# Performance work log

Hardware: AMD Instinct MI355X
Metric: run time of the kernel (lower is better)

The kernel has to match this reference:

```python
import jax, jax.numpy as jnp
import numpy as np


def setup_inputs() -> dict:
    key = jax.random.key(0)
    k1, k2, k3 = jax.random.split(key, 3)
    L, B, H = 256, 8, 512
    inputs = jax.random.normal(k1, (L, B, H), dtype=jnp.float32)
    attn_W = jax.random.normal(k2, (H, 2 * H), dtype=jnp.float32) * 0.02
    attn_b = jnp.zeros((H,), dtype=jnp.float32)
    score_W = jax.random.normal(k3, (1, H), dtype=jnp.float32) * 0.02
    score_b = jnp.zeros((1,), dtype=jnp.float32)
    return {"inputs": inputs, "attn_W": attn_W, "attn_b": attn_b,
            "score_W": score_W, "score_b": score_b}


def reference(inputs, attn_W, attn_b, score_W, score_b):
    # inputs: [L, B, H]; attn_W: [H, 2H] (torch Linear weight), attn_b: [H]
    # score_W: [1, H], score_b: [1]
    H = attn_W.shape[0]
    # Decompose Linear(cat(sen1, sen2)) = sen1 @ W1^T + sen2 @ W2^T + b
    W1 = attn_W[:, :H]   # [H, H] acts on sen1 (row index i)
    W2 = attn_W[:, H:]   # [H, H] acts on sen2 (col index j)
    x = jnp.transpose(inputs, (1, 0, 2))          # [B, L, H]
    p1 = jnp.einsum('blh,oh->blo', x, W1)         # [B, L, H]
    p2 = jnp.einsum('blh,oh->blo', x, W2)         # [B, L, H]
    # feat[b,i,j,:] = tanh(attn(cat(x[b,i], x[b,j])))  -> [B, L, L, H]
    feat = jnp.tanh(p1[:, :, None, :] + p2[:, None, :, :] + attn_b)
    # score Linear H -> 1, squeeze last dim -> [B, L, L]
    energies = jnp.einsum('bijh,h->bij', feat, score_W[0]) + score_b[0]
    # softmax over dim=1 (the sen1 / i axis), as in the torch code
    return jax.nn.softmax(energies, axis=1)
```

## Files before the change

kernel.cpp:

```cpp
#include <hip/hip_runtime.h>

#define LOG2E 1.4426950408889634f
#define SCALE (2.0f * LOG2E)

__device__ __forceinline__ float fast_exp2(float x) { return __builtin_amdgcn_exp2f(x); }
__device__ __forceinline__ float fast_rcp(float x)  { return __builtin_amdgcn_rcpf(x); }

typedef __attribute__((ext_vector_type(8))) short bf16x8;
typedef __attribute__((ext_vector_type(4))) float f32x4;

__global__ __launch_bounds__(256) void pack_kernel(const float* __restrict__ inputs,
                                                   const float* __restrict__ attn_W,
                                                   ushort* __restrict__ Ap,
                                                   ushort* __restrict__ Bp) {
    int tid = blockIdx.x * 256 + threadIdx.x;
    const bool isA = tid < 393216;
    int f = isA ? tid : tid - 393216;
    int l  = f & 63;
    int fr = (f >> 6) & 3;
    int ks = (f >> 8) & 1;
    int rem = f >> 9;
    int kt = rem % 24, tb = rem / 24;
    int kp = kt * 64 + ks * 32 + (l >> 4) * 8;
    int seg = kp >> 9, k = kp & 511;
    const float* src;
    bool useLo;
    if (isA) {
        int m = tb * 64 + fr * 16 + (l & 15);
        src = inputs + ((m & 255) * 8 + (m >> 8)) * 512 + k;
        useLo = (seg == 1);
    } else {
        int n = tb * 64 + fr * 16 + (l & 15);
        src = attn_W + (n & 511) * 1024 + (n >> 9) * 512 + k;
        useLo = (seg == 2);
    }
    float4 v0 = *(const float4*)src;
    float4 v1 = *(const float4*)(src + 4);
    float vv[8] = {v0.x, v0.y, v0.z, v0.w, v1.x, v1.y, v1.z, v1.w};
    ushort o[8];
#pragma unroll
    for (int j = 0; j < 8; ++j) {
        unsigned u = __float_as_uint(vv[j]);
        unsigned hi = (u + 0x7FFF + ((u >> 16) & 1)) >> 16;
        if (useLo) {
            float lo = vv[j] - __uint_as_float(hi << 16);
            unsigned ul = __float_as_uint(lo);
            o[j] = (ushort)((ul + 0x7FFF + ((ul >> 16) & 1)) >> 16);
        } else {
            o[j] = (ushort)hi;
        }
    }
    ushort* dst = (isA ? Ap : Bp) + (long)f * 8;
    *(uint4*)dst = *(const uint4*)o;
}

__global__ __launch_bounds__(256) void mfma_gemm(const ushort* __restrict__ Ap,
                                                 const ushort* __restrict__ Bp,
                                                 const float* __restrict__ attn_b,
                                                 float* __restrict__ E1,
                                                 float* __restrict__ E2) {
    const int mb = blockIdx.x & 15;
    const int nb = blockIdx.x >> 4;
    __shared__ ushort lds[2][12288];

    const int t = threadIdx.x;
    const int lane = t & 63, w = t >> 6;
    const int wr = w >> 1, wc = w & 1;

    const ushort* A0 = Ap + (long)(mb * 2 + 0) * 24 * 4096;
    const ushort* A1 = Ap + (long)(mb * 2 + 1) * 24 * 4096;
    const ushort* B0 = Bp + (long)nb * 24 * 4096;

    f32x4 acc[4][2];
#pragma unroll
    for (int i = 0; i < 4; ++i)
#pragma unroll
        for (int j = 0; j < 2; ++j)
            acc[i][j] = (f32x4){0.f, 0.f, 0.f, 0.f};

    uint4 st[6];
    st[0] = ((const uint4*)A0)[t];       st[1] = ((const uint4*)A0)[t + 256];
    st[2] = ((const uint4*)A1)[t];       st[3] = ((const uint4*)A1)[t + 256];
    st[4] = ((const uint4*)B0)[t];       st[5] = ((const uint4*)B0)[t + 256];
#pragma unroll
    for (int r = 0; r < 6; ++r) ((uint4*)lds[0])[t + r * 256] = st[r];
    __syncthreads();

    for (int kt = 0; kt < 24; ++kt) {
        if (kt < 23) {
            const uint4* a0 = (const uint4*)(A0 + (kt + 1) * 4096);
            const uint4* a1 = (const uint4*)(A1 + (kt + 1) * 4096);
            const uint4* b0 = (const uint4*)(B0 + (kt + 1) * 4096);
            st[0] = a0[t]; st[1] = a0[t + 256];
            st[2] = a1[t]; st[3] = a1[t + 256];
            st[4] = b0[t]; st[5] = b0[t + 256];
        }
        const ushort* buf = lds[kt & 1];
#pragma unroll
        for (int ks = 0; ks < 2; ++ks) {
            bf16x8 a[4], b[2];
#pragma unroll
            for (int mf = 0; mf < 4; ++mf)
                a[mf] = *(const bf16x8*)&buf[wr * 4096 + ks * 2048 + mf * 512 + lane * 8];
#pragma unroll
            for (int nn = 0; nn < 2; ++nn)
                b[nn] = *(const bf16x8*)&buf[8192 + ks * 2048 + (wc * 2 + nn) * 512 + lane * 8];
#pragma unroll
            for (int mf = 0; mf < 4; ++mf)
#pragma unroll
                for (int nn = 0; nn < 2; ++nn)
                    acc[mf][nn] = __builtin_amdgcn_mfma_f32_16x16x32_bf16(
                        a[mf], b[nn], acc[mf][nn], 0, 0, 0);
        }
        if (kt < 23) {
            ushort* nbuf = lds[(kt + 1) & 1];
#pragma unroll
            for (int r = 0; r < 6; ++r) ((uint4*)nbuf)[t + r * 256] = st[r];
            __syncthreads();
        }
    }

    const bool isE1 = (nb < 8);
    float* dst = isE1 ? E1 : E2;
    const int b = mb >> 1;
#pragma unroll
    for (int nn = 0; nn < 2; ++nn) {
        int n = nb * 64 + wc * 32 + nn * 16 + (lane & 15);
        int o = n & 511;
        float bias = isE1 ? attn_b[o] : 0.0f;
#pragma unroll
        for (int mf = 0; mf < 4; ++mf) {
            int ti = (mb & 1) * 4 + wr * 2 + (mf >> 1);
            int iibase = (mf & 1) * 16 + (lane >> 4) * 4;
            long rowoff = ((long)(b * 8 + ti) * 512 + o) * 32 + iibase;
#pragma unroll
            for (int r = 0; r < 4; ++r)
                dst[rowoff + r] = fast_exp2(SCALE * (acc[mf][nn][r] + bias));
        }
    }
}

__global__ __launch_bounds__(256) void energy_kernel(const float* __restrict__ E1,
                                                     const float* __restrict__ E2,
                                                     const float* __restrict__ sW,
                                                     float* __restrict__ EP) {
    const int bid = blockIdx.x;
    const int s  = bid & 3;
    const int tj = (bid >> 2) & 7;
    const int ti = (bid >> 5) & 7;
    const int b  = bid >> 8;
    __shared__ float p1s[64 * 32];
    __shared__ float p2s[64 * 32];
    __shared__ float csh[128];

    const int t = threadIdx.x;
    const int tx = t & 15, ty = t >> 4;

    if (t < 128) csh[t] = 2.0f * sW[s * 128 + t];

    const float* p1base = E1 + ((long)(b * 8 + ti) * 512 + s * 128) * 32;
    const float* p2base = E2 + ((long)(b * 8 + tj) * 512 + s * 128) * 32;

    float acc00 = 0.f, acc01 = 0.f, acc10 = 0.f, acc11 = 0.f;

    for (int c0 = 0; c0 < 128; c0 += 64) {
        __syncthreads();
        const float4* s1 = (const float4*)(p1base + c0 * 32);
        const float4* s2 = (const float4*)(p2base + c0 * 32);
        float4* d1 = (float4*)p1s;
        float4* d2 = (float4*)p2s;
        d1[t] = s1[t];  d1[256 + t] = s1[256 + t];
        d2[t] = s2[t];  d2[256 + t] = s2[256 + t];
        __syncthreads();
#pragma unroll 8
        for (int hh = 0; hh < 64; ++hh) {
            float c = csh[c0 + hh];
            float2 a  = *(const float2*)&p1s[hh * 32 + ty * 2];
            float2 bj = *(const float2*)&p2s[hh * 32 + tx * 2];
            acc00 = fmaf(c, fast_rcp(fmaf(a.x, bj.x, 1.0f)), acc00);
            acc01 = fmaf(c, fast_rcp(fmaf(a.x, bj.y, 1.0f)), acc01);
            acc10 = fmaf(c, fast_rcp(fmaf(a.y, bj.x, 1.0f)), acc10);
            acc11 = fmaf(c, fast_rcp(fmaf(a.y, bj.y, 1.0f)), acc11);
        }
    }

    float* Eb = EP + (long)s * 524288 + (long)b * 65536 + (ti * 32) * 256 + tj * 32;
    *(float2*)&Eb[(ty * 2 + 0) * 256 + tx * 2] = make_float2(acc00, acc01);
    *(float2*)&Eb[(ty * 2 + 1) * 256 + tx * 2] = make_float2(acc10, acc11);
}

__global__ __launch_bounds__(256) void softmax_kernel(const float* __restrict__ P0,
                                                      const float* __restrict__ P1,
                                                      const float* __restrict__ P2,
                                                      const float* __restrict__ P3,
                                                      float* __restrict__ out) {
    const int b  = blockIdx.x >> 4;
    const int jt = blockIdx.x & 15;
    const int t  = threadIdx.x;
    const int jx = t & 15;
    const int iy = t >> 4;
    const long base = (long)b * 65536 + jt * 16 + jx;

    float v[16];
#pragma unroll
    for (int k = 0; k < 16; ++k) {
        long idx = base + (long)(iy + k * 16) * 256;
        v[k] = -(P0[idx] + P1[idx] + P2[idx] + P3[idx]);
    }

    float m = v[0];
#pragma unroll
    for (int k = 1; k < 16; ++k) m = fmaxf(m, v[k]);

    __shared__ float red[256];
    red[t] = m;
    __syncthreads();
    if (t < 128) red[t] = fmaxf(red[t], red[t + 128]);
    __syncthreads();
    if (t < 64) red[t] = fmaxf(red[t], red[t + 64]);
    __syncthreads();
    if (t < 32) red[t] = fmaxf(red[t], red[t + 32]);
    __syncthreads();
    if (t < 16) red[t] = fmaxf(red[t], red[t + 16]);
    __syncthreads();
    m = red[jx];
    __syncthreads();

    float ssum = 0.f;
#pragma unroll
    for (int k = 0; k < 16; ++k) {
        v[k] = fast_exp2((v[k] - m) * LOG2E);
        ssum += v[k];
    }
    red[t] = ssum;
    __syncthreads();
    if (t < 128) red[t] += red[t + 128];
    __syncthreads();
    if (t < 64) red[t] += red[t + 64];
    __syncthreads();
    if (t < 32) red[t] += red[t + 32];
    __syncthreads();
    if (t < 16) red[t] += red[t + 16];
    __syncthreads();
    float inv = fast_rcp(red[jx]);

#pragma unroll
    for (int k = 0; k < 16; ++k) {
        long idx = base + (long)(iy + k * 16) * 256;
        out[idx] = v[k] * inv;
    }
}

extern "C" void kernel_launch(void* const* d_in, const int* in_sizes, int n_in,
                              void* d_out, int out_size, void* d_ws, size_t ws_size,
                              hipStream_t stream) {
    const float* inputs  = (const float*)d_in[0];
    const float* attn_W  = (const float*)d_in[1];
    const float* attn_b  = (const float*)d_in[2];
    const float* score_W = (const float*)d_in[3];
    float* out = (float*)d_out;

    float* ws = (float*)d_ws;
    float* E1 = ws;
    float* E2 = ws + (1 << 20);
    float* EP = ws + (2 << 20);
    ushort* Ap = (ushort*)(ws + (4 << 20));
    ushort* Bp = Ap + 3145728;

    pack_kernel<<<2304, 256, 0, stream>>>(inputs, attn_W, Ap, Bp);
    mfma_gemm<<<256, 256, 0, stream>>>(Ap, Bp, attn_b, E1, E2);
    energy_kernel<<<2048, 256, 0, stream>>>(E1, E2, score_W, EP);
    softmax_kernel<<<128, 256, 0, stream>>>(EP, EP + 524288, EP + 2 * 524288,
                                            EP + 3 * 524288, out);
}
```

Before: 64.23 us.

## Combine four reciprocals into one in energy kernel with larger 4x4 register tiles

The energy kernel now puts four rational terms c/(1+ab) over a common denominator, so each group of four hidden units needs a single reciprocal instead of four. It also computes a 4x4 output micro-tile per thread with packed float2 math. Shared memory is transposed and padded, and the hidden dimension is split into 8 partial slices instead of 4, which means the softmax kernel now sums 8 partial buffers. The aim is to ease the transcendental-unit bottleneck, with the risks of possible overflow or precision loss in the product denominators and more partial-sum traffic.

```diff
diff --git a/kernel.cpp b/kernel.cpp
--- a/kernel.cpp
+++ b/kernel.cpp
@@ -8,6 +8,8 @@
 
 typedef __attribute__((ext_vector_type(8))) short bf16x8;
 typedef __attribute__((ext_vector_type(4))) float f32x4;
+typedef __attribute__((ext_vector_type(2))) float f32x2;
+#define F2(u,v) ((f32x2){(u),(v)})
 
 __global__ __launch_bounds__(256) void pack_kernel(const float* __restrict__ inputs,
                                                    const float* __restrict__ attn_W,
@@ -145,54 +147,88 @@
                                                      const float* __restrict__ sW,
                                                      float* __restrict__ EP) {
     const int bid = blockIdx.x;
-    const int s  = bid & 3;
-    const int tj = (bid >> 2) & 7;
-    const int ti = (bid >> 5) & 7;
-    const int b  = bid >> 8;
-    __shared__ float p1s[64 * 32];
-    __shared__ float p2s[64 * 32];
-    __shared__ float csh[128];
+    const int tj = bid & 3;
+    const int ti = (bid >> 2) & 3;
+    const int b  = (bid >> 4) & 7;
+    const int s  = bid >> 7;
+    __shared__ float As[64 * 33];
+    __shared__ float Bs[64 * 33];
+    __shared__ float csh[64];
 
     const int t = threadIdx.x;
     const int tx = t & 15, ty = t >> 4;
-
-    if (t < 128) csh[t] = 2.0f * sW[s * 128 + t];
-
-    const float* p1base = E1 + ((long)(b * 8 + ti) * 512 + s * 128) * 32;
-    const float* p2base = E2 + ((long)(b * 8 + tj) * 512 + s * 128) * 32;
-
-    float acc00 = 0.f, acc01 = 0.f, acc10 = 0.f, acc11 = 0.f;
-
-    for (int c0 = 0; c0 < 128; c0 += 64) {
+    if (t < 64) csh[t] = 2.0f * sW[s * 64 + t];
+
+    const int oo = t & 31, iig = t >> 5;
+    const float* a_src = E1 + (long)(b * 8 + ti * 2 + (iig >> 2)) * 16384 + (iig & 3) * 8;
+    const float* b_src = E2 + (long)(b * 8 + tj * 2 + (iig >> 2)) * 16384 + (iig & 3) * 8;
+
+    f32x2 acc[4][2];
+#pragma unroll
+    for (int r = 0; r < 4; ++r)
+#pragma unroll
+        for (int cp = 0; cp < 2; ++cp) acc[r][cp] = F2(0.f, 0.f);
+
+    const f32x2 one = F2(1.f, 1.f);
+
+    for (int st = 0; st < 2; ++st) {
+        const long ob = (long)(s * 64 + st * 32 + oo) * 32;
+        float4 va0 = *(const float4*)(a_src + ob);
+        float4 va1 = *(const float4*)(a_src + ob + 4);
+        float4 vb0 = *(const float4*)(b_src + ob);
+        float4 vb1 = *(const float4*)(b_src + ob + 4);
         __syncthreads();
-        const float4* s1 = (const float4*)(p1base + c0 * 32);
-        const float4* s2 = (const float4*)(p2base + c0 * 32);
-        float4* d1 = (float4*)p1s;
-        float4* d2 = (float4*)p2s;
-        d1[t] = s1[t];  d1[256 + t] = s1[256 + t];
-        d2[t] = s2[t];  d2[256 + t] = s2[256 + t];
+        const int di = iig * 8;
+        As[(di + 0) * 33 + oo] = va0.x; As[(di + 1) * 33 + oo] = va0.y;
+        As[(di + 2) * 33 + oo] = va0.z; As[(di + 3) * 33 + oo] = va0.w;
+        As[(di + 4) * 33 + oo] = va1.x; As[(di + 5) * 33 + oo] = va1.y;
+        As[(di + 6) * 33 + oo] = va1.z; As[(di + 7) * 33 + oo] = va1.w;
+        Bs[(di + 0) * 33 + oo] = vb0.x; Bs[(di + 1) * 33 + oo] = vb0.y;
+        Bs[(di + 2) * 33 + oo] = vb0.z; Bs[(di + 3) * 33 + oo] = vb0.w;
+        Bs[(di + 4) * 33 + oo] = vb1.x; Bs[(di + 5) * 33 + oo] = vb1.y;
+        Bs[(di + 6) * 33 + oo] = vb1.z; Bs[(di + 7) * 33 + oo] = vb1.w;
         __syncthreads();
-#pragma unroll 8
-        for (int hh = 0; hh < 64; ++hh) {
-            float c = csh[c0 + hh];
-            float2 a  = *(const float2*)&p1s[hh * 32 + ty * 2];
-            float2 bj = *(const float2*)&p2s[hh * 32 + tx * 2];
-            acc00 = fmaf(c, fast_rcp(fmaf(a.x, bj.x, 1.0f)), acc00);
-            acc01 = fmaf(c, fast_rcp(fmaf(a.x, bj.y, 1.0f)), acc01);
-            acc10 = fmaf(c, fast_rcp(fmaf(a.y, bj.x, 1.0f)), acc10);
-            acc11 = fmaf(c, fast_rcp(fmaf(a.y, bj.y, 1.0f)), acc11);
-        }
-    }
-
-    float* Eb = EP + (long)s * 524288 + (long)b * 65536 + (ti * 32) * 256 + tj * 32;
-    *(float2*)&Eb[(ty * 2 + 0) * 256 + tx * 2] = make_float2(acc00, acc01);
-    *(float2*)&Eb[(ty * 2 + 1) * 256 + tx * 2] = make_float2(acc10, acc11);
-}
-
-__global__ __launch_bounds__(256) void softmax_kernel(const float* __restrict__ P0,
-                                                      const float* __restrict__ P1,
-                                                      const float* __restrict__ P2,
-                                                      const float* __restrict__ P3,
+
+#pragma unroll
+        for (int g = 0; g < 8; ++g) {
+            float4 c4 = *(const float4*)&csh[st * 32 + g * 4];
+            float4 av[4], bv[4];
+#pragma unroll
+            for (int r = 0; r < 4; ++r)
+                av[r] = *(const float4*)&As[(ty * 4 + r) * 33 + g * 4];
+#pragma unroll
+            for (int c = 0; c < 4; ++c)
+                bv[c] = *(const float4*)&Bs[(tx * 4 + c) * 33 + g * 4];
+#pragma unroll
+            for (int r = 0; r < 4; ++r) {
+#pragma unroll
+                for (int cp = 0; cp < 2; ++cp) {
+                    const float4 B0 = bv[cp * 2], B1 = bv[cp * 2 + 1];
+                    f32x2 y0 = F2(B0.x, B1.x) * av[r].x + one;
+                    f32x2 y1 = F2(B0.y, B1.y) * av[r].y + one;
+                    f32x2 y2 = F2(B0.z, B1.z) * av[r].z + one;
+                    f32x2 y3 = F2(B0.w, B1.w) * av[r].w + one;
+                    f32x2 y01 = y0 * y1, y23 = y2 * y3;
+                    f32x2 d = y01 * y23;
+                    f32x2 n01 = y1 * c4.x + y0 * c4.y;
+                    f32x2 n23 = y3 * c4.z + y2 * c4.w;
+                    f32x2 n = n01 * y23 + n23 * y01;
+                    f32x2 rr = F2(fast_rcp(d.x), fast_rcp(d.y));
+                    acc[r][cp] += n * rr;
+                }
+            }
+        }
+    }
+
+    float* Eb = EP + (long)s * 524288 + (long)b * 65536 + (long)(ti * 64) * 256 + tj * 64;
+#pragma unroll
+    for (int r = 0; r < 4; ++r)
+#pragma unroll
+        for (int cp = 0; cp < 2; ++cp)
+            *(f32x2*)&Eb[(ty * 4 + r) * 256 + tx * 4 + cp * 2] = acc[r][cp];
+}
+
+__global__ __launch_bounds__(256) void softmax_kernel(const float* __restrict__ EP,
                                                       float* __restrict__ out) {
     const int b  = blockIdx.x >> 4;
     const int jt = blockIdx.x & 15;
@@ -205,7 +241,10 @@
 #pragma unroll
     for (int k = 0; k < 16; ++k) {
         long idx = base + (long)(iy + k * 16) * 256;
-        v[k] = -(P0[idx] + P1[idx] + P2[idx] + P3[idx]);
+        float sum = 0.f;
+#pragma unroll
+        for (int p = 0; p < 8; ++p) sum += EP[(long)p * 524288 + idx];
+        v[k] = -sum;
     }
 
     float m = v[0];
@@ -264,12 +303,11 @@
     float* E1 = ws;
     float* E2 = ws + (1 << 20);
     float* EP = ws + (2 << 20);
-    ushort* Ap = (ushort*)(ws + (4 << 20));
+    ushort* Ap = (ushort*)(ws + (6 << 20));
     ushort* Bp = Ap + 3145728;
 
     pack_kernel<<<2304, 256, 0, stream>>>(inputs, attn_W, Ap, Bp);
     mfma_gemm<<<256, 256, 0, stream>>>(Ap, Bp, attn_b, E1, E2);
-    energy_kernel<<<2048, 256, 0, stream>>>(E1, E2, score_W, EP);
-    softmax_kernel<<<128, 256, 0, stream>>>(EP, EP + 524288, EP + 2 * 524288,
-                                            EP + 3 * 524288, out);
-}
+    energy_kernel<<<1024, 256, 0, stream>>>(E1, E2, score_W, EP);
+    softmax_kernel<<<128, 256, 0, stream>>>(EP, out);
+}
```

Measured after the change: 86.56 us. 1.35x slower.

## Drop LDS staging in GEMM; stream fragments directly to registers with triple buffering

Applied to the files above, without the earlier changes.

Each wavefront in the bf16 MFMA GEMM now works independently and loads its pre-packed A and B fragments straight from global memory into registers. A three-stage register ring prefetches two k-steps ahead, replacing the shared-memory double buffer and its block barriers. The block-to-tile mapping is also remapped across the grid. This removes LDS traffic and __syncthreads stalls, but gives up reuse of tiles across wavefronts, so global and L2 load traffic goes up and register pressure rises.

```diff
diff --git a/kernel.cpp b/kernel.cpp
--- a/kernel.cpp
+++ b/kernel.cpp
@@ -59,17 +59,14 @@
                                                  const float* __restrict__ attn_b,
                                                  float* __restrict__ E1,
                                                  float* __restrict__ E2) {
-    const int mb = blockIdx.x & 15;
-    const int nb = blockIdx.x >> 4;
-    __shared__ ushort lds[2][12288];
-
-    const int t = threadIdx.x;
-    const int lane = t & 63, w = t >> 6;
-    const int wr = w >> 1, wc = w & 1;
-
-    const ushort* A0 = Ap + (long)(mb * 2 + 0) * 24 * 4096;
-    const ushort* A1 = Ap + (long)(mb * 2 + 1) * 24 * 4096;
-    const ushort* B0 = Bp + (long)nb * 24 * 4096;
+    const int lb = (blockIdx.x & 7) * 32 + (blockIdx.x >> 3);
+    const int w = (lb << 2) | (threadIdx.x >> 6);
+    const int lane = threadIdx.x & 63;
+    const int mt  = w >> 5;
+    const int nt2 = w & 31;
+
+    const ushort* pa = Ap + (long)mt * 98304 + lane * 8;
+    const ushort* pb = Bp + (long)(nt2 >> 1) * 98304 + (nt2 & 1) * 1024 + lane * 8;
 
     f32x4 acc[4][2];
 #pragma unroll
@@ -78,61 +75,49 @@
         for (int j = 0; j < 2; ++j)
             acc[i][j] = (f32x4){0.f, 0.f, 0.f, 0.f};
 
-    uint4 st[6];
-    st[0] = ((const uint4*)A0)[t];       st[1] = ((const uint4*)A0)[t + 256];
-    st[2] = ((const uint4*)A1)[t];       st[3] = ((const uint4*)A1)[t + 256];
-    st[4] = ((const uint4*)B0)[t];       st[5] = ((const uint4*)B0)[t + 256];
-#pragma unroll
-    for (int r = 0; r < 6; ++r) ((uint4*)lds[0])[t + r * 256] = st[r];
-    __syncthreads();
-
-    for (int kt = 0; kt < 24; ++kt) {
-        if (kt < 23) {
-            const uint4* a0 = (const uint4*)(A0 + (kt + 1) * 4096);
-            const uint4* a1 = (const uint4*)(A1 + (kt + 1) * 4096);
-            const uint4* b0 = (const uint4*)(B0 + (kt + 1) * 4096);
-            st[0] = a0[t]; st[1] = a0[t + 256];
-            st[2] = a1[t]; st[3] = a1[t + 256];
-            st[4] = b0[t]; st[5] = b0[t + 256];
-        }
-        const ushort* buf = lds[kt & 1];
-#pragma unroll
-        for (int ks = 0; ks < 2; ++ks) {
-            bf16x8 a[4], b[2];
-#pragma unroll
-            for (int mf = 0; mf < 4; ++mf)
-                a[mf] = *(const bf16x8*)&buf[wr * 4096 + ks * 2048 + mf * 512 + lane * 8];
+    bf16x8 bufA[3][4], bufB[3][2];
+#define LOADK(kk, s)                                              \
+    {                                                             \
+        const ushort* qa = pa + (kk) * 2048;                      \
+        const ushort* qb = pb + (kk) * 2048;                      \
+        bufA[s][0] = *(const bf16x8*)qa;                          \
+        bufA[s][1] = *(const bf16x8*)(qa + 512);                  \
+        bufA[s][2] = *(const bf16x8*)(qa + 1024);                 \
+        bufA[s][3] = *(const bf16x8*)(qa + 1536);                 \
+        bufB[s][0] = *(const bf16x8*)qb;                          \
+        bufB[s][1] = *(const bf16x8*)(qb + 512);                  \
+    }
+
+    LOADK(0, 0);
+    LOADK(1, 1);
+#pragma unroll 3
+    for (int kk = 0; kk < 48; ++kk) {
+        const int cur = kk % 3;
+        if (kk < 46) {
+            const int nxt = (kk + 2) % 3;
+            LOADK(kk + 2, nxt);
+        }
+#pragma unroll
+        for (int mf = 0; mf < 4; ++mf)
 #pragma unroll
             for (int nn = 0; nn < 2; ++nn)
-                b[nn] = *(const bf16x8*)&buf[8192 + ks * 2048 + (wc * 2 + nn) * 512 + lane * 8];
-#pragma unroll
-            for (int mf = 0; mf < 4; ++mf)
-#pragma unroll
-                for (int nn = 0; nn < 2; ++nn)
-                    acc[mf][nn] = __builtin_amdgcn_mfma_f32_16x16x32_bf16(
-                        a[mf], b[nn], acc[mf][nn], 0, 0, 0);
-        }
-        if (kt < 23) {
-            ushort* nbuf = lds[(kt + 1) & 1];
-#pragma unroll
-            for (int r = 0; r < 6; ++r) ((uint4*)nbuf)[t + r * 256] = st[r];
-            __syncthreads();
-        }
-    }
-
-    const bool isE1 = (nb < 8);
+                acc[mf][nn] = __builtin_amdgcn_mfma_f32_16x16x32_bf16(
+                    bufA[cur][mf], bufB[cur][nn], acc[mf][nn], 0, 0, 0);
+    }
+#undef LOADK
+
+    const bool isE1 = (nt2 < 16);
     float* dst = isE1 ? E1 : E2;
-    const int b = mb >> 1;
 #pragma unroll
     for (int nn = 0; nn < 2; ++nn) {
-        int n = nb * 64 + wc * 32 + nn * 16 + (lane & 15);
+        int n = nt2 * 32 + nn * 16 + (lane & 15);
         int o = n & 511;
         float bias = isE1 ? attn_b[o] : 0.0f;
 #pragma unroll
         for (int mf = 0; mf < 4; ++mf) {
-            int ti = (mb & 1) * 4 + wr * 2 + (mf >> 1);
-            int iibase = (mf & 1) * 16 + (lane >> 4) * 4;
-            long rowoff = ((long)(b * 8 + ti) * 512 + o) * 32 + iibase;
+            int ml = mt * 64 + mf * 16 + ((lane >> 4) << 2);
+            int bb = ml >> 8, l = ml & 255;
+            long rowoff = ((long)(bb * 8 + (l >> 5)) * 512 + o) * 32 + (l & 31);
 #pragma unroll
             for (int r = 0; r < 4; ++r)
                 dst[rowoff + r] = fast_exp2(SCALE * (acc[mf][nn][r] + bias));
```

New measurement: 67.57 us. 5.2% more time.

## Enlarge GEMM block tile to 256x128 with 8 waves per block

Applied to the files above, without the earlier changes.

The bf16 MFMA GEMM now uses 512-thread blocks that each compute a 256x128 output tile, instead of 256-thread blocks computing 128x64 tiles. The grid shrinks from 256 blocks to 64. Each wave accumulates a 64x64 sub-tile, which raises data reuse per LDS load and cuts the total global traffic for A and B. In exchange, only 64 blocks run on a GPU with many more compute units, so most of the device sits idle, and register and LDS use per block roughly double.

```diff
diff --git a/kernel.cpp b/kernel.cpp
--- a/kernel.cpp
+++ b/kernel.cpp
@@ -54,88 +54,97 @@
     *(uint4*)dst = *(const uint4*)o;
 }
 
-__global__ __launch_bounds__(256) void mfma_gemm(const ushort* __restrict__ Ap,
+__global__ __launch_bounds__(512) void mfma_gemm(const ushort* __restrict__ Ap,
                                                  const ushort* __restrict__ Bp,
                                                  const float* __restrict__ attn_b,
                                                  float* __restrict__ E1,
                                                  float* __restrict__ E2) {
-    const int mb = blockIdx.x & 15;
-    const int nb = blockIdx.x >> 4;
-    __shared__ ushort lds[2][12288];
+    const int mt = blockIdx.x & 7;
+    const int nb = blockIdx.x >> 3;
+    __shared__ ushort lds[2][24576];
 
     const int t = threadIdx.x;
     const int lane = t & 63, w = t >> 6;
-    const int wr = w >> 1, wc = w & 1;
-
-    const ushort* A0 = Ap + (long)(mb * 2 + 0) * 24 * 4096;
-    const ushort* A1 = Ap + (long)(mb * 2 + 1) * 24 * 4096;
-    const ushort* B0 = Bp + (long)nb * 24 * 4096;
-
-    f32x4 acc[4][2];
+    const int wrm = w >> 1, wcn = w & 1;
+
+    const ushort* aBase = Ap + (long)(mt * 4) * 98304;
+    const ushort* bBase = Bp + (long)(nb * 2) * 98304;
+
+    f32x4 acc[4][4];
 #pragma unroll
     for (int i = 0; i < 4; ++i)
 #pragma unroll
-        for (int j = 0; j < 2; ++j)
+        for (int j = 0; j < 4; ++j)
             acc[i][j] = (f32x4){0.f, 0.f, 0.f, 0.f};
 
     uint4 st[6];
-    st[0] = ((const uint4*)A0)[t];       st[1] = ((const uint4*)A0)[t + 256];
-    st[2] = ((const uint4*)A1)[t];       st[3] = ((const uint4*)A1)[t + 256];
-    st[4] = ((const uint4*)B0)[t];       st[5] = ((const uint4*)B0)[t + 256];
-#pragma unroll
-    for (int r = 0; r < 6; ++r) ((uint4*)lds[0])[t + r * 256] = st[r];
+#define LOADK(kt)                                                              \
+    {                                                                          \
+        st[0] = *(const uint4*)(aBase + 0 * 98304 + (kt) * 4096 + t * 8);      \
+        st[1] = *(const uint4*)(aBase + 1 * 98304 + (kt) * 4096 + t * 8);      \
+        st[2] = *(const uint4*)(aBase + 2 * 98304 + (kt) * 4096 + t * 8);      \
+        st[3] = *(const uint4*)(aBase + 3 * 98304 + (kt) * 4096 + t * 8);      \
+        st[4] = *(const uint4*)(bBase + 0 * 98304 + (kt) * 4096 + t * 8);      \
+        st[5] = *(const uint4*)(bBase + 1 * 98304 + (kt) * 4096 + t * 8);      \
+    }
+#define STOREK(buf)                                                            \
+    {                                                                          \
+        ushort* d = lds[buf];                                                  \
+        *(uint4*)(d + 0 * 4096 + t * 8) = st[0];                               \
+        *(uint4*)(d + 1 * 4096 + t * 8) = st[1];                               \
+        *(uint4*)(d + 2 * 4096 + t * 8) = st[2];                               \
+        *(uint4*)(d + 3 * 4096 + t * 8) = st[3];                               \
+        *(uint4*)(d + 4 * 4096 + t * 8) = st[4];                               \
+        *(uint4*)(d + 5 * 4096 + t * 8) = st[5];                               \
+    }
+
+    LOADK(0);
+    STOREK(0);
     __syncthreads();
 
     for (int kt = 0; kt < 24; ++kt) {
+        const int cur = kt & 1;
+        if (kt < 23) LOADK(kt + 1);
+        const ushort* buf = lds[cur];
+#pragma unroll
+        for (int ks = 0; ks < 2; ++ks) {
+            bf16x8 a[4], b[4];
+#pragma unroll
+            for (int mf = 0; mf < 4; ++mf)
+                a[mf] = *(const bf16x8*)&buf[wrm * 4096 + ks * 2048 + mf * 512 + lane * 8];
+#pragma unroll
+            for (int nf = 0; nf < 4; ++nf)
+                b[nf] = *(const bf16x8*)&buf[(4 + wcn) * 4096 + ks * 2048 + nf * 512 + lane * 8];
+#pragma unroll
+            for (int mf = 0; mf < 4; ++mf)
+#pragma unroll
+                for (int nf = 0; nf < 4; ++nf)
+                    acc[mf][nf] = __builtin_amdgcn_mfma_f32_16x16x32_bf16(
+                        a[mf], b[nf], acc[mf][nf], 0, 0, 0);
+        }
         if (kt < 23) {
-            const uint4* a0 = (const uint4*)(A0 + (kt + 1) * 4096);
-            const uint4* a1 = (const uint4*)(A1 + (kt + 1) * 4096);
-            const uint4* b0 = (const uint4*)(B0 + (kt + 1) * 4096);
-            st[0] = a0[t]; st[1] = a0[t + 256];
-            st[2] = a1[t]; st[3] = a1[t + 256];
-            st[4] = b0[t]; st[5] = b0[t + 256];
-        }
-        const ushort* buf = lds[kt & 1];
-#pragma unroll
-        for (int ks = 0; ks < 2; ++ks) {
-            bf16x8 a[4], b[2];
-#pragma unroll
-            for (int mf = 0; mf < 4; ++mf)
-                a[mf] = *(const bf16x8*)&buf[wr * 4096 + ks * 2048 + mf * 512 + lane * 8];
-#pragma unroll
-            for (int nn = 0; nn < 2; ++nn)
-                b[nn] = *(const bf16x8*)&buf[8192 + ks * 2048 + (wc * 2 + nn) * 512 + lane * 8];
-#pragma unroll
-            for (int mf = 0; mf < 4; ++mf)
-#pragma unroll
-                for (int nn = 0; nn < 2; ++nn)
-                    acc[mf][nn] = __builtin_amdgcn_mfma_f32_16x16x32_bf16(
-                        a[mf], b[nn], acc[mf][nn], 0, 0, 0);
-        }
-        if (kt < 23) {
-            ushort* nbuf = lds[(kt + 1) & 1];
-#pragma unroll
-            for (int r = 0; r < 6; ++r) ((uint4*)nbuf)[t + r * 256] = st[r];
-            __syncthreads();
-        }
-    }
-
-    const bool isE1 = (nb < 8);
-    float* dst = isE1 ? E1 : E2;
-    const int b = mb >> 1;
-#pragma unroll
-    for (int nn = 0; nn < 2; ++nn) {
-        int n = nb * 64 + wc * 32 + nn * 16 + (lane & 15);
+            STOREK(cur ^ 1);
+        }
+        __syncthreads();
+    }
+#undef LOADK
+#undef STOREK
+
+#pragma unroll
+    for (int nf = 0; nf < 4; ++nf) {
+        int n = nb * 128 + wcn * 64 + nf * 16 + (lane & 15);
+        const bool isE1 = (n < 512);
+        float* dst = isE1 ? E1 : E2;
         int o = n & 511;
         float bias = isE1 ? attn_b[o] : 0.0f;
 #pragma unroll
         for (int mf = 0; mf < 4; ++mf) {
-            int ti = (mb & 1) * 4 + wr * 2 + (mf >> 1);
-            int iibase = (mf & 1) * 16 + (lane >> 4) * 4;
-            long rowoff = ((long)(b * 8 + ti) * 512 + o) * 32 + iibase;
+            int ml = mt * 256 + wrm * 64 + mf * 16 + ((lane >> 4) << 2);
+            int bb = ml >> 8, l = ml & 255;
+            long rowoff = ((long)(bb * 8 + (l >> 5)) * 512 + o) * 32 + (l & 31);
 #pragma unroll
             for (int r = 0; r < 4; ++r)
-                dst[rowoff + r] = fast_exp2(SCALE * (acc[mf][nn][r] + bias));
+                dst[rowoff + r] = fast_exp2(SCALE * (acc[mf][nf][r] + bias));
         }
     }
 }
@@ -268,7 +277,7 @@
     ushort* Bp = Ap + 3145728;
 
     pack_kernel<<<2304, 256, 0, stream>>>(inputs, attn_W, Ap, Bp);
-    mfma_gemm<<<256, 256, 0, stream>>>(Ap, Bp, attn_b, E1, E2);
+    mfma_gemm<<<64, 512, 0, stream>>>(Ap, Bp, attn_b, E1, E2);
     energy_kernel<<<2048, 256, 0, stream>>>(E1, E2, score_W, EP);
     softmax_kernel<<<128, 256, 0, stream>>>(EP, EP + 524288, EP + 2 * 524288,
                                             EP + 3 * 524288, out);
```

Measured after the change: 75.98 us. 1.18x slower.
